# Kernel optimization log

Measured on AMD Instinct MI355X. Metric: run time of the kernel, lower is better.

## Reference

```python
import jax, jax.numpy as jnp
import numpy as np

NEG_SLOPE = 0.05

def _leaky(v):
    return jnp.where(v >= 0, v, NEG_SLOPE * v)

def setup_inputs() -> dict:
    key = jax.random.key(0)
    ks = jax.random.split(key, 9)
    B, N, D = 8, 96, 16
    H0, H1, OUT = 50, 50, 64
    x = jax.random.normal(ks[0], (B, N, D), dtype=jnp.float32)
    # dense 0/1 adjacency (float, used directly in matmuls), avg degree ~ 0.15*N
    adj = (jax.random.uniform(ks[1], (B, N, N)) < 0.15).astype(jnp.float32)
    h1 = 3 * D + 3          # 51
    h2 = 2 * D + H0 + 1     # 83
    h3 = D + H1             # 66
    W1 = jax.random.normal(ks[2], (h1, H0), dtype=jnp.float32) / np.sqrt(h1)
    b1 = jax.random.normal(ks[3], (H0,), dtype=jnp.float32) * 0.01
    W2 = jax.random.normal(ks[4], (h2, H1), dtype=jnp.float32) / np.sqrt(h2)
    b2 = jax.random.normal(ks[5], (H1,), dtype=jnp.float32) * 0.01
    W3 = jax.random.normal(ks[6], (h3, OUT), dtype=jnp.float32) / np.sqrt(h3)
    b3 = jax.random.normal(ks[7], (OUT,), dtype=jnp.float32) * 0.01
    return {"x": x, "adj": adj, "W1": W1, "b1": b1, "W2": W2, "b2": b2, "W3": W3, "b3": b3}

def reference(x, adj, W1, b1, W2, b2, W3, b3):
    # Faithful math of SpatialGraphConv.forward, with the O(N^4)/O(N^3)
    # broadcast+concat+GEMM algebraically decomposed into O(N^2) einsums
    # (identical result: the concat-GEMM is a sum of per-block contributions).
    B, N, D = x.shape
    H0 = W1.shape[1]
    # pairwise distances dis[b,i,j]
    diff = x[:, :, None, :] - x[:, None, :, :]            # (B,N,N,D)
    dis = jnp.sqrt(jnp.sum(diff * diff, axis=-1) + 1e-10)  # (B,N,N)
    # split W1 rows per concat block [x_i | x_j | x_k | d_ij | d_jk | d_ik]
    Wxi, Wxj, Wxk = W1[:D], W1[D:2 * D], W1[2 * D:3 * D]
    w_ij, w_jk, w_ik = W1[3 * D], W1[3 * D + 1], W1[3 * D + 2]  # (H0,)
    A = x @ Wxi   # (B,N,H0), indexed by i
    Bm = x @ Wxj  # (B,N,H0), indexed by j
    C = x @ Wxk   # (B,N,H0), indexed by k
    # m3_sum[b,i,j,h] = adj[b,i,j] * sum_k adj[b,j,k] * m3pre[b,i,j,k,h]
    deg = jnp.sum(adj, axis=-1)                           # (B,N): sum_k adj[b,j,k]
    sumC = jnp.einsum('bjk,bkh->bjh', adj, C)             # (B,N,H0)
    sd_jk = jnp.sum(adj * dis, axis=-1)                   # (B,N): sum_k adj[j,k]*dis[j,k]
    sd_ik = jnp.einsum('bik,bjk->bij', dis, adj)          # (B,N,N): sum_k adj[j,k]*dis[i,k]
    S = (deg[:, None, :, None] * (A[:, :, None, :] + Bm[:, None, :, :] + b1
                                   + dis[..., None] * w_ij)
         + sumC[:, None, :, :]
         + sd_jk[:, None, :, None] * w_jk
         + sd_ik[..., None] * w_ik)                        # (B,N,N,H0)
    m3_sum = _leaky(adj[..., None] * S)                    # (B,N,N,H0)
    # stage 2: pairwise concat [x_i | x_j | dis | m3_sum] -> MLP -> adj-masked sum over j
    xi = jnp.broadcast_to(x[:, :, None, :], (B, N, N, D))
    xj = jnp.broadcast_to(x[:, None, :, :], (B, N, N, D))
    feat2 = jnp.concatenate([xi, xj, dis[..., None], m3_sum], axis=-1)  # (B,N,N,2D+1+H0)
    m2 = feat2 @ W2 + b2                                   # (B,N,N,H1)
    m2_sum = _leaky(jnp.einsum('bijh,bij->bih', m2, adj))  # (B,N,H1)
    # stage 3: node-wise MLP
    m1 = _leaky(jnp.concatenate([x, m2_sum], axis=-1) @ W3 + b3)  # (B,N,OUT)
    return m1
```

## Files before the change

kernel.cpp:

```cpp
#include <hip/hip_runtime.h>
#include <math.h>

#define BB   8
#define NN   96
#define DD   16
#define H0D  50
#define H1D  50
#define OUTD 64
#define XPAD 17
#define APAD 97


__global__ __launch_bounds__(128) void k1_precompute(
    const float* __restrict__ x, const float* __restrict__ adj,
    const float* __restrict__ W1,
    float* __restrict__ dis, float* __restrict__ deg, float* __restrict__ sdjk,
    float* __restrict__ nx, float* __restrict__ A, float* __restrict__ Bm,
    float* __restrict__ sumC)
{
    const int b = blockIdx.x / NN, r = blockIdx.x % NN;
    const int tid = threadIdx.x;
    __shared__ float sx[NN * XPAD];
    __shared__ float sadj[NN];
    __shared__ float sdis[NN];
    __shared__ float snx[DD];

    for (int idx = tid; idx < NN * DD; idx += 128)
        sx[(idx / DD) * XPAD + (idx % DD)] = x[b * NN * DD + idx];
    if (tid < NN) sadj[tid] = adj[(b * NN + r) * NN + tid];
    __syncthreads();

    if (tid < NN) {
        float s = 1e-10f;
        #pragma unroll
        for (int d = 0; d < DD; ++d) {
            float t = sx[r * XPAD + d] - sx[tid * XPAD + d];
            s += t * t;
        }
        float dv = sqrtf(s);
        sdis[tid] = dv;
        dis[(b * NN + r) * NN + tid] = dv;
    }
    __syncthreads();

    if (tid < DD) {
        float s = 0.f;
        for (int k = 0; k < NN; ++k) s += sadj[k] * sx[k * XPAD + tid];
        snx[tid] = s;
        nx[(b * NN + r) * DD + tid] = s;
    } else if (tid == DD) {
        float s = 0.f;
        for (int k = 0; k < NN; ++k) s += sadj[k];
        deg[b * NN + r] = s;
    } else if (tid == DD + 1) {
        float s = 0.f;
        for (int k = 0; k < NN; ++k) s += sadj[k] * sdis[k];
        sdjk[b * NN + r] = s;
    }
    __syncthreads();

    if (tid < H0D) {
        float a = 0.f, bm = 0.f, sc = 0.f;
        #pragma unroll
        for (int d = 0; d < DD; ++d) {
            float xr = sx[r * XPAD + d];
            a  += xr * W1[d * H0D + tid];
            bm += xr * W1[(DD + d) * H0D + tid];
            sc += snx[d] * W1[(2 * DD + d) * H0D + tid];
        }
        int o = (b * NN + r) * H0D + tid;
        A[o] = a; Bm[o] = bm; sumC[o] = sc;
    }
}

__global__ __launch_bounds__(128) void k2_main(
    const float* __restrict__ x, const float* __restrict__ adj,
    const float* __restrict__ W1, const float* __restrict__ b1,
    const float* __restrict__ W2, const float* __restrict__ b2,
    const float* __restrict__ W3, const float* __restrict__ b3,
    const float* __restrict__ dis, const float* __restrict__ deg,
    const float* __restrict__ sdjk, const float* __restrict__ nx,
    const float* __restrict__ A, const float* __restrict__ Bm,
    const float* __restrict__ sumC, float* __restrict__ out)
{
    const int b = blockIdx.x / NN, i = blockIdx.x % NN;
    const int tid = threadIdx.x;
    __shared__ float sAdj[NN * APAD];
    __shared__ float sdis[NN];
    __shared__ float sdik[NN];
    __shared__ float sagg[96];
    __shared__ float sm2s[H1D];

    for (int idx = tid; idx < NN * NN; idx += 128)
        sAdj[(idx / NN) * APAD + (idx % NN)] = adj[b * NN * NN + idx];
    if (tid < NN) sdis[tid] = dis[(b * NN + i) * NN + tid];
    __syncthreads();

    if (tid < NN) {
        float s = 0.f;
        const float* row = &sAdj[tid * APAD];
        for (int k = 0; k < NN; ++k) s += sdis[k] * row[k];
        sdik[tid] = s;
    }
    __syncthreads();

    float msum = 0.f;
    float a_ih = 0.f, b1h = 0.f, wij = 0.f, wjk = 0.f, wik = 0.f;
    if (tid < H0D) {
        a_ih = A[(b * NN + i) * H0D + tid];
        b1h = b1[tid];
        wij = W1[(3 * DD + 0) * H0D + tid];
        wjk = W1[(3 * DD + 1) * H0D + tid];
        wik = W1[(3 * DD + 2) * H0D + tid];
    }
    for (int j = 0; j < NN; ++j) {
        float aij = sAdj[i * APAD + j];
        if (aij == 0.f) continue;
        if (tid < H0D) {
            float degj  = deg[b * NN + j];
            float sdjkj = sdjk[b * NN + j];
            float bmjh = Bm[(b * NN + j) * H0D + tid];
            float scjh = sumC[(b * NN + j) * H0D + tid];
            float S = degj * (a_ih + bmjh + b1h + sdis[j] * wij)
                    + scjh + sdjkj * wjk + sdik[j] * wik;
            float v = aij * S;
            v = (v >= 0.f) ? v : 0.05f * v;
            msum += aij * v;
        }
    }

    float degi = deg[b * NN + i];
    if (tid < H0D) sagg[33 + tid] = msum;
    if (tid < DD) sagg[tid] = degi * x[(b * NN + i) * DD + tid];
    else if (tid < 2 * DD) sagg[tid] = nx[(b * NN + i) * DD + (tid - DD)];
    else if (tid == 2 * DD) sagg[tid] = sdjk[b * NN + i];
    __syncthreads();

    if (tid < H1D) {
        float s = degi * b2[tid];
        for (int c = 0; c < 2 * DD + H0D + 1; ++c)
            s += sagg[c] * W2[c * H1D + tid];
        s = (s >= 0.f) ? s : 0.05f * s;
        sm2s[tid] = s;
    }
    __syncthreads();

    if (tid < OUTD) {
        float s = b3[tid];
        #pragma unroll
        for (int d = 0; d < DD; ++d)
            s += x[(b * NN + i) * DD + d] * W3[d * OUTD + tid];
        for (int h = 0; h < H1D; ++h)
            s += sm2s[h] * W3[(DD + h) * OUTD + tid];
        s = (s >= 0.f) ? s : 0.05f * s;
        out[(b * NN + i) * OUTD + tid] = s;
    }
}

extern "C" void kernel_launch(void* const* d_in, const int* in_sizes, int n_in,
                              void* d_out, int out_size, void* d_ws, size_t ws_size,
                              hipStream_t stream) {
    const float* x   = (const float*)d_in[0];
    const float* adj = (const float*)d_in[1];
    const float* W1  = (const float*)d_in[2];
    const float* b1  = (const float*)d_in[3];
    const float* W2  = (const float*)d_in[4];
    const float* b2  = (const float*)d_in[5];
    const float* W3  = (const float*)d_in[6];
    const float* b3  = (const float*)d_in[7];
    float* out = (float*)d_out;

    float* ws   = (float*)d_ws;
    float* dis  = ws;
    float* deg  = dis + BB * NN * NN;
    float* sdjk = deg + BB * NN;
    float* nx   = sdjk + BB * NN;
    float* A    = nx + BB * NN * DD;
    float* Bm   = A + BB * NN * H0D;
    float* sumC = Bm + BB * NN * H0D;

    k1_precompute<<<BB * NN, 128, 0, stream>>>(x, adj, W1, dis, deg, sdjk, nx, A, Bm, sumC);
    k2_main<<<BB * NN, 128, 0, stream>>>(x, adj, W1, b1, W2, b2, W3, b3,
                                         dis, deg, sdjk, nx, A, Bm, sumC, out);
}
```

Measured before the change: 92.58 us.

## Fuse both kernels into one tiled kernel using adjacency bitmasks

Replaces the two-kernel pipeline with one kernel in which each block handles 16 rows of one batch and recomputes per-batch quantities (degrees, neighbour sums, distance sums) in shared memory. Adjacency rows are packed into 64-bit ballot masks so sparse sums iterate only over set bits, and the Bm/sumC terms are folded into one precomputed per-j table. This removes the global-memory round trip, the second launch and the full adjacency copy into shared memory per row. The cost is far fewer blocks (48) and redundant per-batch precompute in each tile, which may leave much of the GPU idle.

```diff
diff --git a/kernel.cpp b/kernel.cpp
--- a/kernel.cpp
+++ b/kernel.cpp
@@ -7,153 +7,175 @@
 #define H0D  50
 #define H1D  50
 #define OUTD 64
-#define XPAD 17
-#define APAD 97
+#define IT   16
+#define TILES 6
+#define XP   17
+#define DP   97
 
 
-__global__ __launch_bounds__(128) void k1_precompute(
-    const float* __restrict__ x, const float* __restrict__ adj,
-    const float* __restrict__ W1,
-    float* __restrict__ dis, float* __restrict__ deg, float* __restrict__ sdjk,
-    float* __restrict__ nx, float* __restrict__ A, float* __restrict__ Bm,
-    float* __restrict__ sumC)
-{
-    const int b = blockIdx.x / NN, r = blockIdx.x % NN;
-    const int tid = threadIdx.x;
-    __shared__ float sx[NN * XPAD];
-    __shared__ float sadj[NN];
-    __shared__ float sdis[NN];
-    __shared__ float snx[DD];
-
-    for (int idx = tid; idx < NN * DD; idx += 128)
-        sx[(idx / DD) * XPAD + (idx % DD)] = x[b * NN * DD + idx];
-    if (tid < NN) sadj[tid] = adj[(b * NN + r) * NN + tid];
-    __syncthreads();
-
-    if (tid < NN) {
-        float s = 1e-10f;
-        #pragma unroll
-        for (int d = 0; d < DD; ++d) {
-            float t = sx[r * XPAD + d] - sx[tid * XPAD + d];
-            s += t * t;
-        }
-        float dv = sqrtf(s);
-        sdis[tid] = dv;
-        dis[(b * NN + r) * NN + tid] = dv;
-    }
-    __syncthreads();
-
-    if (tid < DD) {
-        float s = 0.f;
-        for (int k = 0; k < NN; ++k) s += sadj[k] * sx[k * XPAD + tid];
-        snx[tid] = s;
-        nx[(b * NN + r) * DD + tid] = s;
-    } else if (tid == DD) {
-        float s = 0.f;
-        for (int k = 0; k < NN; ++k) s += sadj[k];
-        deg[b * NN + r] = s;
-    } else if (tid == DD + 1) {
-        float s = 0.f;
-        for (int k = 0; k < NN; ++k) s += sadj[k] * sdis[k];
-        sdjk[b * NN + r] = s;
-    }
-    __syncthreads();
-
-    if (tid < H0D) {
-        float a = 0.f, bm = 0.f, sc = 0.f;
-        #pragma unroll
-        for (int d = 0; d < DD; ++d) {
-            float xr = sx[r * XPAD + d];
-            a  += xr * W1[d * H0D + tid];
-            bm += xr * W1[(DD + d) * H0D + tid];
-            sc += snx[d] * W1[(2 * DD + d) * H0D + tid];
-        }
-        int o = (b * NN + r) * H0D + tid;
-        A[o] = a; Bm[o] = bm; sumC[o] = sc;
-    }
-}
-
-__global__ __launch_bounds__(128) void k2_main(
+__global__ __launch_bounds__(256) void sgc_fused(
     const float* __restrict__ x, const float* __restrict__ adj,
     const float* __restrict__ W1, const float* __restrict__ b1,
     const float* __restrict__ W2, const float* __restrict__ b2,
     const float* __restrict__ W3, const float* __restrict__ b3,
-    const float* __restrict__ dis, const float* __restrict__ deg,
-    const float* __restrict__ sdjk, const float* __restrict__ nx,
-    const float* __restrict__ A, const float* __restrict__ Bm,
-    const float* __restrict__ sumC, float* __restrict__ out)
+    float* __restrict__ out)
 {
-    const int b = blockIdx.x / NN, i = blockIdx.x % NN;
-    const int tid = threadIdx.x;
-    __shared__ float sAdj[NN * APAD];
-    __shared__ float sdis[NN];
-    __shared__ float sdik[NN];
-    __shared__ float sagg[96];
-    __shared__ float sm2s[H1D];
+    const int b  = blockIdx.x / TILES;
+    const int i0 = (blockIdx.x % TILES) * IT;
+    const int tid  = threadIdx.x;
+    const int wv   = tid >> 6;
+    const int lane = tid & 63;
 
-    for (int idx = tid; idx < NN * NN; idx += 128)
-        sAdj[(idx / NN) * APAD + (idx % NN)] = adj[b * NN * NN + idx];
-    if (tid < NN) sdis[tid] = dis[(b * NN + i) * NN + tid];
+    __shared__ float sx[NN * XP];
+    __shared__ unsigned long long smask[NN][2];
+    __shared__ float snx[NN * XP];
+    __shared__ float sdeg[NN], ssdjk[NN];
+    __shared__ float sP[NN * H0D];
+    __shared__ float sA[IT * H0D];
+    __shared__ float sdisI[IT * DP];
+    __shared__ float ssdik[IT * DP];
+    __shared__ float smsum[IT * H0D];
+    __shared__ float sm2s[IT * H1D];
+
+    for (int t = tid; t < NN * DD; t += 256)
+        sx[(t >> 4) * XP + (t & 15)] = x[(size_t)b * NN * DD + t];
+    for (int j = wv; j < NN; j += 4) {
+        const float* arow = adj + ((size_t)b * NN + j) * NN;
+        unsigned long long m0 = __ballot(arow[lane] != 0.f);
+        float v1 = (lane < NN - 64) ? arow[64 + lane] : 0.f;
+        unsigned long long m1 = __ballot(v1 != 0.f);
+        if (lane == 0) { smask[j][0] = m0; smask[j][1] = m1; }
+    }
     __syncthreads();
 
     if (tid < NN) {
+        const int j = tid;
+        unsigned long long m0 = smask[j][0], m1 = smask[j][1];
+        float dg = (float)(__popcll(m0) + __popcll(m1));
+        float sd = 0.f;
+        const float* xj = &sx[j * XP];
+        unsigned long long mm = m0; int base = 0;
+        for (int half = 0; half < 2; ++half) {
+            while (mm) {
+                int k = base + __ffsll((unsigned long long)mm) - 1;
+                mm &= mm - 1;
+                const float* xk = &sx[k * XP];
+                float s = 1e-10f;
+                #pragma unroll
+                for (int d = 0; d < DD; ++d) { float t = xj[d] - xk[d]; s += t * t; }
+                sd += sqrtf(s);
+            }
+            mm = m1; base = 64;
+        }
+        sdeg[j] = dg; ssdjk[j] = sd;
+    }
+    for (int t = tid; t < NN * DD; t += 256) {
+        int j = t >> 4, d = t & 15;
+        unsigned long long m0 = smask[j][0], m1 = smask[j][1];
         float s = 0.f;
-        const float* row = &sAdj[tid * APAD];
-        for (int k = 0; k < NN; ++k) s += sdis[k] * row[k];
-        sdik[tid] = s;
+        while (m0) { int k = __ffsll((unsigned long long)m0) - 1; m0 &= m0 - 1; s += sx[k * XP + d]; }
+        while (m1) { int k = 64 + __ffsll((unsigned long long)m1) - 1; m1 &= m1 - 1; s += sx[k * XP + d]; }
+        snx[j * XP + d] = s;
+    }
+    for (int t = tid; t < IT * H0D; t += 256) {
+        int ii = t / H0D, h = t % H0D;
+        const float* xi = &sx[(i0 + ii) * XP];
+        float s = 0.f;
+        #pragma unroll
+        for (int d = 0; d < DD; ++d) s += xi[d] * W1[d * H0D + h];
+        sA[t] = s;
+    }
+    for (int t = tid; t < IT * NN; t += 256) {
+        int ii = t / NN, k = t % NN;
+        const float* xi = &sx[(i0 + ii) * XP];
+        const float* xk = &sx[k * XP];
+        float s = 1e-10f;
+        #pragma unroll
+        for (int d = 0; d < DD; ++d) { float tt = xi[d] - xk[d]; s += tt * tt; }
+        sdisI[ii * DP + k] = sqrtf(s);
     }
     __syncthreads();
 
-    float msum = 0.f;
-    float a_ih = 0.f, b1h = 0.f, wij = 0.f, wjk = 0.f, wik = 0.f;
-    if (tid < H0D) {
-        a_ih = A[(b * NN + i) * H0D + tid];
-        b1h = b1[tid];
-        wij = W1[(3 * DD + 0) * H0D + tid];
-        wjk = W1[(3 * DD + 1) * H0D + tid];
-        wik = W1[(3 * DD + 2) * H0D + tid];
+    for (int t = tid; t < NN * H0D; t += 256) {
+        int j = t / H0D, h = t % H0D;
+        float dg = sdeg[j];
+        const float* xj = &sx[j * XP];
+        const float* nj = &snx[j * XP];
+        float s = 0.f;
+        #pragma unroll
+        for (int d = 0; d < DD; ++d)
+            s += dg * xj[d] * W1[(DD + d) * H0D + h] + nj[d] * W1[(2 * DD + d) * H0D + h];
+        sP[t] = s;
     }
-    for (int j = 0; j < NN; ++j) {
-        float aij = sAdj[i * APAD + j];
-        if (aij == 0.f) continue;
-        if (tid < H0D) {
-            float degj  = deg[b * NN + j];
-            float sdjkj = sdjk[b * NN + j];
-            float bmjh = Bm[(b * NN + j) * H0D + tid];
-            float scjh = sumC[(b * NN + j) * H0D + tid];
-            float S = degj * (a_ih + bmjh + b1h + sdis[j] * wij)
-                    + scjh + sdjkj * wjk + sdik[j] * wik;
-            float v = aij * S;
-            v = (v >= 0.f) ? v : 0.05f * v;
-            msum += aij * v;
-        }
-    }
-
-    float degi = deg[b * NN + i];
-    if (tid < H0D) sagg[33 + tid] = msum;
-    if (tid < DD) sagg[tid] = degi * x[(b * NN + i) * DD + tid];
-    else if (tid < 2 * DD) sagg[tid] = nx[(b * NN + i) * DD + (tid - DD)];
-    else if (tid == 2 * DD) sagg[tid] = sdjk[b * NN + i];
-    __syncthreads();
-
-    if (tid < H1D) {
-        float s = degi * b2[tid];
-        for (int c = 0; c < 2 * DD + H0D + 1; ++c)
-            s += sagg[c] * W2[c * H1D + tid];
-        s = (s >= 0.f) ? s : 0.05f * s;
-        sm2s[tid] = s;
+    for (int t = tid; t < IT * NN; t += 256) {
+        int ii = t / NN, j = t % NN;
+        unsigned long long m0 = smask[j][0], m1 = smask[j][1];
+        const float* di = &sdisI[ii * DP];
+        float s = 0.f;
+        while (m0) { int k = __ffsll((unsigned long long)m0) - 1; m0 &= m0 - 1; s += di[k]; }
+        while (m1) { int k = 64 + __ffsll((unsigned long long)m1) - 1; m1 &= m1 - 1; s += di[k]; }
+        ssdik[ii * DP + j] = s;
     }
     __syncthreads();
 
-    if (tid < OUTD) {
-        float s = b3[tid];
+    const int hl = (lane < H0D) ? lane : 0;
+    float b1l = 0.f, wij = 0.f, wjk = 0.f, wik = 0.f;
+    if (lane < H0D) {
+        b1l = b1[lane];
+        wij = W1[(3 * DD + 0) * H0D + lane];
+        wjk = W1[(3 * DD + 1) * H0D + lane];
+        wik = W1[(3 * DD + 2) * H0D + lane];
+    }
+    for (int r = 0; r < IT / 4; ++r) {
+        const int ii = r * 4 + wv;
+        const int i  = i0 + ii;
+        const float ab = sA[ii * H0D + hl] + b1l;
+        float msum = 0.f;
+        unsigned long long mm = smask[i][0]; int base = 0;
+        for (int half = 0; half < 2; ++half) {
+            while (mm) {
+                int j = base + __ffsll((unsigned long long)mm) - 1;
+                mm &= mm - 1;
+                float S = sdeg[j] * (ab + sdisI[ii * DP + j] * wij)
+                        + sP[j * H0D + hl]
+                        + ssdjk[j] * wjk + ssdik[ii * DP + j] * wik;
+                msum += (S >= 0.f) ? S : 0.05f * S;
+            }
+            mm = smask[i][1]; base = 64;
+        }
+        if (lane < H0D) smsum[ii * H0D + lane] = msum;
+    }
+    __syncthreads();
+
+    for (int t = tid; t < IT * H1D; t += 256) {
+        int ii = t / H1D, h = t % H1D;
+        int i = i0 + ii;
+        float dg = sdeg[i];
+        float s = dg * b2[h];
+        const float* xi = &sx[i * XP];
+        const float* ni = &snx[i * XP];
         #pragma unroll
         for (int d = 0; d < DD; ++d)
-            s += x[(b * NN + i) * DD + d] * W3[d * OUTD + tid];
-        for (int h = 0; h < H1D; ++h)
-            s += sm2s[h] * W3[(DD + h) * OUTD + tid];
+            s += dg * xi[d] * W2[d * H1D + h] + ni[d] * W2[(DD + d) * H1D + h];
+        s += ssdjk[i] * W2[(2 * DD) * H1D + h];
+        const float* ms = &smsum[ii * H0D];
+        for (int c = 0; c < H0D; ++c)
+            s += ms[c] * W2[(2 * DD + 1 + c) * H1D + h];
+        sm2s[t] = (s >= 0.f) ? s : 0.05f * s;
+    }
+    __syncthreads();
+
+    for (int t = tid; t < IT * OUTD; t += 256) {
+        int ii = t >> 6, o = t & 63;
+        int i = i0 + ii;
+        float s = b3[o];
+        const float* xi = &sx[i * XP];
+        #pragma unroll
+        for (int d = 0; d < DD; ++d) s += xi[d] * W3[d * OUTD + o];
+        const float* m2 = &sm2s[ii * H1D];
+        for (int h = 0; h < H1D; ++h) s += m2[h] * W3[(DD + h) * OUTD + o];
         s = (s >= 0.f) ? s : 0.05f * s;
-        out[(b * NN + i) * OUTD + tid] = s;
+        out[((size_t)(b * NN + i)) * OUTD + o] = s;
     }
 }
 
@@ -170,16 +192,5 @@
     const float* b3  = (const float*)d_in[7];
     float* out = (float*)d_out;
 
-    float* ws   = (float*)d_ws;
-    float* dis  = ws;
-    float* deg  = dis + BB * NN * NN;
-    float* sdjk = deg + BB * NN;
-    float* nx   = sdjk + BB * NN;
-    float* A    = nx + BB * NN * DD;
-    float* Bm   = A + BB * NN * H0D;
-    float* sumC = Bm + BB * NN * H0D;
-
-    k1_precompute<<<BB * NN, 128, 0, stream>>>(x, adj, W1, dis, deg, sdjk, nx, A, Bm, sumC);
-    k2_main<<<BB * NN, 128, 0, stream>>>(x, adj, W1, b1, W2, b2, W3, b3,
-                                         dis, deg, sdjk, nx, A, Bm, sumC, out);
+    sgc_fused<<<BB * TILES, 256, 0, stream>>>(x, adj, W1, b1, W2, b2, W3, b3, out);
 }
```

Result: slower. 131.0 us (+41.5%).
